# Optimization experiments

Hardware: AMD Instinct MI355X
Metric: run time of the kernel (lower is better)

Reference implementation:

```python
import jax, jax.numpy as jnp
import numpy as np

D_MODEL = 2048
N_HEADS = 8
HEAD_DIM = D_MODEL // N_HEADS
SCALING = HEAD_DIM ** -0.5


def setup_inputs() -> dict:
    key = jax.random.key(0)
    ks = jax.random.split(key, 9)
    B, S, D = 2, 2048, D_MODEL
    std = D ** -0.5
    inp = {"x": jax.random.normal(ks[0], (B, S, D), dtype=jnp.float32)}
    names = ["Wq", "Wk", "Wv", "Wo"]
    for i, n in enumerate(names):
        inp[n] = jax.random.normal(ks[1 + i], (D, D), dtype=jnp.float32) * std
        inp["b" + n[1]] = jax.random.normal(ks[5 + i], (D,), dtype=jnp.float32) * 0.01
    return inp


def reference(x, Wq, bq, Wk, bk, Wv, bv, Wo, bo):
    B, S, D = x.shape
    H, hd = N_HEADS, HEAD_DIM

    def proj(W, b):
        # nn.Linear: x @ W.T + b, then split heads -> [B, H, S, hd]
        y = jnp.einsum("bsd,ed->bse", x, W) + b
        return y.reshape(B, S, H, hd).transpose(0, 2, 1, 3)

    q = proj(Wq, bq)
    k = proj(Wk, bk)
    v = proj(Wv, bv)

    # scaled QK^T: [B, H, S, S]
    attn_weights = jnp.einsum("bhqd,bhkd->bhqk", q, k) * SCALING
    causal = jnp.tril(jnp.ones((S, S), dtype=bool))  # [S, S]
    attn_weights = jnp.where(causal[None, None], attn_weights, -jnp.inf)
    attn_probs = jax.nn.softmax(attn_weights, axis=-1)

    out = jnp.einsum("bhqk,bhkd->bhqd", attn_probs, v)  # [B, H, S, hd]
    out = out.transpose(0, 2, 1, 3).reshape(B, S, D)
    out = jnp.einsum("bsd,ed->bse", out, Wo) + bo
    return (out, attn_probs)
```

## Files before the change

kernel.cpp:

```cpp
#include <hip/hip_runtime.h>
#include <cstdint>
#include <cstddef>

typedef _Float16 f16;
typedef __attribute__((ext_vector_type(4))) _Float16 f16x4;
typedef __attribute__((ext_vector_type(8))) _Float16 f16x8;
typedef __attribute__((ext_vector_type(4))) float f32x4;

#define NB 2
#define SEQ 2048
#define DM 2048
#define NH 8
#define HD 256
#define MT (NB * SEQ)

#define QSCALE 0.09016844f
#define CEXP   23.08312065f

__device__ __forceinline__ void gload16(const f16* g, f16* l) {
    __builtin_amdgcn_global_load_lds(
        (const __attribute__((address_space(1))) uint32_t*)(const void*)g,
        (__attribute__((address_space(3))) uint32_t*)(void*)l,
        16, 0, 0);
}

__global__ __launch_bounds__(256) void k_cvt(const float* __restrict__ src,
                                             f16* __restrict__ dst, int n) {
    for (int i = (blockIdx.x * blockDim.x + threadIdx.x) * 4; i < n;
         i += gridDim.x * blockDim.x * 4) {
        f32x4 v = *(const f32x4*)(src + i);
        f16x4 h;
        h[0] = (f16)v[0]; h[1] = (f16)v[1]; h[2] = (f16)v[2]; h[3] = (f16)v[3];
        *(f16x4*)(dst + i) = h;
    }
}

__device__ __forceinline__ void stage6(const f16* __restrict__ A,
                                       const f16* __restrict__ B,
                                       int m0, int n0, int k0,
                                       f16* AL, f16* BL, int tid) {
#pragma unroll
    for (int j = 0; j < 4; ++j) {
        int flat = j * 4096 + tid * 8;
        int r = flat >> 6, c = flat & 63;
        int cs = c ^ ((r & 7) << 3);
        gload16(A + (size_t)(m0 + r) * DM + k0 + cs,
                AL + j * 4096 + (tid >> 6) * 512);
    }
#pragma unroll
    for (int j = 0; j < 2; ++j) {
        int flat = j * 4096 + tid * 8;
        int r = flat >> 6, c = flat & 63;
        int cs = c ^ ((r & 7) << 3);
        gload16(B + (size_t)(n0 + r) * DM + k0 + cs,
                BL + j * 4096 + (tid >> 6) * 512);
    }
}

__device__ __forceinline__ f16x8 rdfrag(const f16* buf, int rowbase, int lr,
                                        int lg, int kk) {
    int row = rowbase + lr;
    int c = (kk * 32 + lg * 8) ^ ((lr & 7) << 3);
    return *(const f16x8*)&buf[row * 64 + c];
}

__device__ __forceinline__ void gemm256x128_core(const f16* __restrict__ A,
                                                 const f16* __restrict__ B,
                                                 int m0, int n0,
                                                 f16* AL, f16* BL,
                                                 f32x4 acc[4][4]) {
    const int tid = threadIdx.x, wave = tid >> 6, lane = tid & 63;
    const int wm = wave >> 1, wn = wave & 1;
    const int lr = lane & 15, lg = lane >> 4;
    const int nt = DM / 64;

    stage6(A, B, m0, n0, 0, AL, BL, tid);
    stage6(A, B, m0, n0, 64, AL + 16384, BL + 8192, tid);

    for (int kt = 0; kt < nt; ++kt) {
        if (kt + 1 < nt) asm volatile("s_waitcnt vmcnt(6)" ::: "memory");
        else             asm volatile("s_waitcnt vmcnt(0)" ::: "memory");
        __builtin_amdgcn_s_barrier();
        __builtin_amdgcn_sched_barrier(0);

        const f16* Ab = AL + (kt % 3) * 16384;
        const f16* Bb = BL + (kt % 3) * 8192;
        const int arb = wm * 64, brb = wn * 64;

        f16x8 a0[2][2], b0[2][2];
#pragma unroll
        for (int mf = 0; mf < 2; ++mf)
#pragma unroll
            for (int kk = 0; kk < 2; ++kk)
                a0[mf][kk] = rdfrag(Ab, arb + mf * 16, lr, lg, kk);
#pragma unroll
        for (int nf = 0; nf < 2; ++nf)
#pragma unroll
            for (int kk = 0; kk < 2; ++kk)
                b0[nf][kk] = rdfrag(Bb, brb + nf * 16, lr, lg, kk);

        if (kt + 2 < nt)
            stage6(A, B, m0, n0, (kt + 2) * 64,
                   AL + ((kt + 2) % 3) * 16384, BL + ((kt + 2) % 3) * 8192, tid);

        __builtin_amdgcn_s_setprio(1);
#pragma unroll
        for (int mi = 0; mi < 2; ++mi)
#pragma unroll
            for (int nj = 0; nj < 2; ++nj)
#pragma unroll
                for (int kk = 0; kk < 2; ++kk)
                    acc[mi][nj] = __builtin_amdgcn_mfma_f32_16x16x32_f16(
                        a0[mi][kk], b0[nj][kk], acc[mi][nj], 0, 0, 0);
        __builtin_amdgcn_s_setprio(0);

        f16x8 b1[2][2];
#pragma unroll
        for (int nf = 0; nf < 2; ++nf)
#pragma unroll
            for (int kk = 0; kk < 2; ++kk)
                b1[nf][kk] = rdfrag(Bb, brb + 32 + nf * 16, lr, lg, kk);
        __builtin_amdgcn_s_setprio(1);
#pragma unroll
        for (int mi = 0; mi < 2; ++mi)
#pragma unroll
            for (int nj = 0; nj < 2; ++nj)
#pragma unroll
                for (int kk = 0; kk < 2; ++kk)
                    acc[mi][nj + 2] = __builtin_amdgcn_mfma_f32_16x16x32_f16(
                        a0[mi][kk], b1[nj][kk], acc[mi][nj + 2], 0, 0, 0);
        __builtin_amdgcn_s_setprio(0);

        f16x8 a1[2][2];
#pragma unroll
        for (int mf = 0; mf < 2; ++mf)
#pragma unroll
            for (int kk = 0; kk < 2; ++kk)
                a1[mf][kk] = rdfrag(Ab, arb + 32 + mf * 16, lr, lg, kk);
        __builtin_amdgcn_s_setprio(1);
#pragma unroll
        for (int mi = 0; mi < 2; ++mi)
#pragma unroll
            for (int nj = 0; nj < 2; ++nj)
#pragma unroll
                for (int kk = 0; kk < 2; ++kk)
                    acc[mi + 2][nj] = __builtin_amdgcn_mfma_f32_16x16x32_f16(
                        a1[mi][kk], b0[nj][kk], acc[mi + 2][nj], 0, 0, 0);
        __builtin_amdgcn_s_setprio(0);

        __builtin_amdgcn_s_setprio(1);
#pragma unroll
        for (int mi = 0; mi < 2; ++mi)
#pragma unroll
            for (int nj = 0; nj < 2; ++nj)
#pragma unroll
                for (int kk = 0; kk < 2; ++kk)
                    acc[mi + 2][nj + 2] = __builtin_amdgcn_mfma_f32_16x16x32_f16(
                        a1[mi][kk], b1[nj][kk], acc[mi + 2][nj + 2], 0, 0, 0);
        __builtin_amdgcn_s_setprio(0);
    }
}

__global__ __launch_bounds__(512, 1) void k_proj_qkv(
    const f16* __restrict__ xh, const f16* __restrict__ Wq,
    const f16* __restrict__ Wk, const f16* __restrict__ Wv,
    const float* __restrict__ bq, const float* __restrict__ bk,
    const float* __restrict__ bv,
    f16* __restrict__ Qh, f16* __restrict__ Kh, f16* __restrict__ Vth) {
    __shared__ __align__(16) f16 AL[3 * 16384];
    __shared__ __align__(16) f16 BL[3 * 8192];
    const int mode = blockIdx.z;
    const f16* W = (mode == 0) ? Wq : (mode == 1) ? Wk : Wv;
    const float* bias = (mode == 0) ? bq : (mode == 1) ? bk : bv;

    const int phys = blockIdx.x + 16 * blockIdx.y;
    const int xcdq = phys & 7, idx = phys >> 3;
    const int m0 = (xcdq * 2 + (idx >> 4)) * 256;
    const int n0 = (idx & 15) * 128;

    f32x4 acc[4][4];
#pragma unroll
    for (int mi = 0; mi < 4; ++mi)
#pragma unroll
        for (int nj = 0; nj < 4; ++nj) acc[mi][nj] = (f32x4){0.f, 0.f, 0.f, 0.f};

    gemm256x128_core(xh, W, m0, n0, AL, BL, acc);

    const int lane = threadIdx.x & 63, wave = threadIdx.x >> 6;
    const int wm = wave >> 1, wn = wave & 1;
    const int lr = lane & 15, lg = lane >> 4;
#pragma unroll
    for (int nj = 0; nj < 4; ++nj) {
        int n = n0 + wn * 64 + nj * 16 + lr;
        float bb = bias[n];
        int h = n >> 8, d = n & 255;
#pragma unroll
        for (int mi = 0; mi < 4; ++mi) {
#pragma unroll
            for (int i = 0; i < 4; ++i) {
                int m = m0 + wm * 64 + mi * 16 + lg * 4 + i;
                int b = m >> 11, s = m & 2047;
                float v = acc[mi][nj][i] + bb;
                size_t bh = (size_t)(b * NH + h);
                if (mode == 0)
                    Qh[((bh * SEQ + s) << 8) + d] = (f16)(v * QSCALE);
                else if (mode == 1)
                    Kh[((bh * SEQ + s) << 8) + d] = (f16)v;
                else
                    Vth[((bh * HD + d) << 11) + s] = (f16)v;
            }
        }
    }
}

__global__ __launch_bounds__(512, 1) void k_proj_o(
    const f16* __restrict__ Oh, const f16* __restrict__ Wo,
    const float* __restrict__ bo, float* __restrict__ out) {
    __shared__ __align__(16) f16 AL[3 * 16384];
    __shared__ __align__(16) f16 BL[3 * 8192];

    const int phys = blockIdx.x + 16 * blockIdx.y;
    const int xcdq = phys & 7, idx = phys >> 3;
    const int m0 = (xcdq * 2 + (idx >> 4)) * 256;
    const int n0 = (idx & 15) * 128;

    f32x4 acc[4][4];
#pragma unroll
    for (int mi = 0; mi < 4; ++mi)
#pragma unroll
        for (int nj = 0; nj < 4; ++nj) acc[mi][nj] = (f32x4){0.f, 0.f, 0.f, 0.f};

    gemm256x128_core(Oh, Wo, m0, n0, AL, BL, acc);

    const int lane = threadIdx.x & 63, wave = threadIdx.x >> 6;
    const int wm = wave >> 1, wn = wave & 1;
    const int lr = lane & 15, lg = lane >> 4;
#pragma unroll
    for (int nj = 0; nj < 4; ++nj) {
        int n = n0 + wn * 64 + nj * 16 + lr;
        float bb = bo[n];
#pragma unroll
        for (int mi = 0; mi < 4; ++mi) {
#pragma unroll
            for (int i = 0; i < 4; ++i) {
                int m = m0 + wm * 64 + mi * 16 + lg * 4 + i;
                out[(size_t)m * DM + n] = acc[mi][nj][i] + bb;
            }
        }
    }
}

__device__ __forceinline__ void stageK(const f16* __restrict__ Kb, int kt,
                                       f16* buf, int wave, int lane) {
#pragma unroll
    for (int j = 0; j < 8; ++j) {
        int base = (j * 4 + wave) << 9;
        int flat = base + (lane << 3);
        int r = flat >> 8;
        int c = (flat & 255) ^ ((r & 7) << 3);
        gload16(Kb + (size_t)(kt * 64 + r) * HD + c, buf + base);
    }
}
__device__ __forceinline__ void stageV(const f16* __restrict__ Vb, int kt,
                                       f16* buf, int wave, int lane) {
#pragma unroll
    for (int j = 0; j < 8; ++j) {
        int base = (j * 4 + wave) << 9;
        int flat = base + (lane << 3);
        int rv = flat >> 6;
        int cv = (flat & 63) ^ ((rv & 3) << 3);
        gload16(Vb + ((size_t)rv << 11) + kt * 64 + cv, buf + base);
    }
}

__global__ __launch_bounds__(256, 2) void k_attn(
    const f16* __restrict__ Qh, const f16* __restrict__ Kh,
    const f16* __restrict__ Vth, float* __restrict__ P,
    f16* __restrict__ Oh) {
    __shared__ __align__(16) f16 B0[64 * 256];
    __shared__ __align__(16) f16 B1[64 * 256];
    __shared__ __align__(16) f16 Ps[4][16][72];

    const int bid = blockIdx.x;
    const int xcd = bid & 7;
    const int slot = bid >> 3;
    const int psel = slot >> 5;
    const int s5 = slot & 31;
    const int qb = psel ? s5 : (31 - s5);
    const int bhid = xcd * 2 + psel;
    const int b = bhid >> 3, h = bhid & 7;

    const int q0 = qb * 64;
    const int tid = threadIdx.x, wave = tid >> 6, lane = tid & 63;
    const int lr = lane & 15, lg = lane >> 4;
    const size_t bh = (size_t)bhid;
    const f16* Qb = Qh + (bh << 19);
    const f16* Kb = Kh + (bh << 19);
    const f16* Vb = Vth + (bh << 19);
    float* Pb = P + (bh << 22);

    const int kswz = (lr & 7) << 3;
    const int vswz = (lr & 3) << 3;

    f16x8 aq[8];
    {
        const f16* qrow = Qb + (size_t)(q0 + wave * 16 + lr) * HD + lg * 8;
#pragma unroll
        for (int kk = 0; kk < 8; ++kk) aq[kk] = *(const f16x8*)(qrow + kk * 32);
    }

    const int rowb = q0 + wave * 16 + lg * 4;
    const int nt = qb + 1;

    float psum[4] = {0.f, 0.f, 0.f, 0.f};

    stageK(Kb, 0, B0, wave, lane);
    for (int kt = 0; kt < nt; ++kt) {
        f16* cur = (kt & 1) ? B1 : B0;
        f16* nxt = (kt & 1) ? B0 : B1;
        if (kt + 1 < nt) {
            stageK(Kb, kt + 1, nxt, wave, lane);
            asm volatile("s_waitcnt vmcnt(8)" ::: "memory");
        } else {
            asm volatile("s_waitcnt vmcnt(0)" ::: "memory");
        }
        __builtin_amdgcn_s_barrier();
        __builtin_amdgcn_sched_barrier(0);

        f32x4 s[4];
#pragma unroll
        for (int nj = 0; nj < 4; ++nj) s[nj] = (f32x4){0.f, 0.f, 0.f, 0.f};
        __builtin_amdgcn_s_setprio(1);
#pragma unroll
        for (int kk = 0; kk < 8; ++kk) {
#pragma unroll
            for (int nj = 0; nj < 4; ++nj) {
                f16x8 bk = *(const f16x8*)&cur[(nj * 16 + lr) * 256 +
                                               ((kk * 32 + lg * 8) ^ kswz)];
                s[nj] = __builtin_amdgcn_mfma_f32_16x16x32_f16(aq[kk], bk, s[nj], 0, 0, 0);
            }
        }
        __builtin_amdgcn_s_setprio(0);
        const int colb = kt * 64 + lr;
#pragma unroll
        for (int i = 0; i < 4; ++i) {
            int row = rowb + i;
#pragma unroll
            for (int nj = 0; nj < 4; ++nj)
                psum[i] += (colb + nj * 16 <= row) ? exp2f(s[nj][i] - CEXP) : 0.f;
        }
        asm volatile("" ::: "memory");
        __builtin_amdgcn_s_barrier();
        __builtin_amdgcn_sched_barrier(0);
    }

    float inv[4];
#pragma unroll
    for (int i = 0; i < 4; ++i) {
        float l = psum[i];
        l += __shfl_xor(l, 1);
        l += __shfl_xor(l, 2);
        l += __shfl_xor(l, 4);
        l += __shfl_xor(l, 8);
        inv[i] = 1.f / l;
    }

    f32x4 o[16];
#pragma unroll
    for (int n = 0; n < 16; ++n) o[n] = (f32x4){0.f, 0.f, 0.f, 0.f};

    stageK(Kb, 0, B0, wave, lane);
    for (int kt = 0; kt < nt; ++kt) {
        stageV(Vb, kt, B1, wave, lane);
        asm volatile("s_waitcnt vmcnt(8)" ::: "memory");
        __builtin_amdgcn_s_barrier();
        __builtin_amdgcn_sched_barrier(0);

        f32x4 s[4];
#pragma unroll
        for (int nj = 0; nj < 4; ++nj) s[nj] = (f32x4){0.f, 0.f, 0.f, 0.f};
        __builtin_amdgcn_s_setprio(1);
#pragma unroll
        for (int kk = 0; kk < 8; ++kk) {
#pragma unroll
            for (int nj = 0; nj < 4; ++nj) {
                f16x8 bk = *(const f16x8*)&B0[(nj * 16 + lr) * 256 +
                                              ((kk * 32 + lg * 8) ^ kswz)];
                s[nj] = __builtin_amdgcn_mfma_f32_16x16x32_f16(aq[kk], bk, s[nj], 0, 0, 0);
            }
        }
        __builtin_amdgcn_s_setprio(0);
#pragma unroll
        for (int i = 0; i < 4; ++i) {
            int row = rowb + i;
#pragma unroll
            for (int nj = 0; nj < 4; ++nj) {
                int col = kt * 64 + nj * 16 + lr;
                float pv = (col <= row) ? exp2f(s[nj][i] - CEXP) * inv[i] : 0.f;
                Ps[wave][lg * 4 + i][nj * 16 + lr] = (f16)pv;
            }
        }
        asm volatile("s_waitcnt vmcnt(0)" ::: "memory");
        __builtin_amdgcn_s_barrier();
        __builtin_amdgcn_sched_barrier(0);

        if (kt + 1 < nt) stageK(Kb, kt + 1, B0, wave, lane);

#pragma unroll
        for (int h2 = 0; h2 < 2; ++h2) {
            int rr = h2 * 8 + (lane >> 3);
            int cc = (lane & 7) * 8;
            f16x8 ph = *(const f16x8*)&Ps[wave][rr][cc];
            int row = q0 + wave * 16 + rr;
            float* dst = Pb + (size_t)row * SEQ + kt * 64 + cc;
            f32x4 lo = {(float)ph[0], (float)ph[1], (float)ph[2], (float)ph[3]};
            f32x4 hi = {(float)ph[4], (float)ph[5], (float)ph[6], (float)ph[7]};
            *(f32x4*)dst = lo;
            *(f32x4*)(dst + 4) = hi;
        }

        __builtin_amdgcn_s_setprio(1);
#pragma unroll
        for (int kk2 = 0; kk2 < 2; ++kk2) {
            f16x8 pa = *(const f16x8*)&Ps[wave][lr][kk2 * 32 + lg * 8];
#pragma unroll
            for (int n = 0; n < 16; ++n) {
                f16x8 bv = *(const f16x8*)&B1[(n * 16 + lr) * 64 +
                                              ((kk2 * 32 + lg * 8) ^ vswz)];
                o[n] = __builtin_amdgcn_mfma_f32_16x16x32_f16(pa, bv, o[n], 0, 0, 0);
            }
        }
        __builtin_amdgcn_s_setprio(0);
        asm volatile("" ::: "memory");
        __builtin_amdgcn_s_barrier();
        __builtin_amdgcn_sched_barrier(0);
    }

    int kstart = (qb + 1) * 64;
    if (kstart < SEQ) {
        f32x4 z = (f32x4){0.f, 0.f, 0.f, 0.f};
        for (int r = 0; r < 64; ++r) {
            float* rp = Pb + (size_t)(q0 + r) * SEQ;
            for (int c = kstart + tid * 4; c < SEQ; c += 1024)
                *(f32x4*)(rp + c) = z;
        }
    }

#pragma unroll
    for (int n = 0; n < 16; ++n) {
#pragma unroll
        for (int i = 0; i < 4; ++i) {
            int row = rowb + i;
            int d = n * 16 + lr;
            Oh[((size_t)b * SEQ + row) * DM + h * HD + d] = (f16)o[n][i];
        }
    }
}

extern "C" void kernel_launch(void* const* d_in, const int* in_sizes, int n_in,
                              void* d_out, int out_size, void* d_ws, size_t ws_size,
                              hipStream_t stream) {
    const float* x  = (const float*)d_in[0];
    const float* Wq = (const float*)d_in[1];
    const float* bq = (const float*)d_in[2];
    const float* Wk = (const float*)d_in[3];
    const float* bk = (const float*)d_in[4];
    const float* Wv = (const float*)d_in[5];
    const float* bv = (const float*)d_in[6];
    const float* Wo = (const float*)d_in[7];
    const float* bo = (const float*)d_in[8];

    float* out  = (float*)d_out;
    float* Pout = out + (size_t)MT * DM;

    f16* xh  = (f16*)Pout;
    f16* Wqh = xh + (size_t)MT * DM;
    f16* Wkh = Wqh + (size_t)DM * DM;
    f16* Wvh = Wkh + (size_t)DM * DM;

    f16* ws16 = (f16*)d_ws;
    f16* Woh = ws16;
    f16* Qh  = Woh + (size_t)DM * DM;
    f16* Kh  = Qh + (size_t)8388608;
    f16* Vth = Kh + (size_t)8388608;
    f16* Oh  = Vth + (size_t)8388608;
    if (ws_size < (size_t)(4194304 + 4 * 8388608) * sizeof(f16)) return;

    k_cvt<<<2048, 256, 0, stream>>>(x, xh, MT * DM);
    k_cvt<<<1024, 256, 0, stream>>>(Wq, Wqh, DM * DM);
    k_cvt<<<1024, 256, 0, stream>>>(Wk, Wkh, DM * DM);
    k_cvt<<<1024, 256, 0, stream>>>(Wv, Wvh, DM * DM);
    k_cvt<<<1024, 256, 0, stream>>>(Wo, Woh, DM * DM);

    dim3 g1(DM / 128, MT / 256, 3);
    k_proj_qkv<<<g1, 512, 0, stream>>>(xh, Wqh, Wkh, Wvh, bq, bk, bv, Qh, Kh, Vth);

    k_attn<<<dim3(512), 256, 0, stream>>>(Qh, Kh, Vth, Pout, Oh);

    dim3 g3(DM / 128, MT / 256, 1);
    k_proj_o<<<g3, 512, 0, stream>>>(Oh, Woh, bo, out);
}
```

Before: 371.9 us.

## Restructure GEMM main loop into two k-phases and reorder PV before P store

The projection GEMM inner loop now runs as two k-half phases. Each phase loads 4x4 fragments, issues half of the next tile's global-to-LDS loads, then runs 16 MFMAs between extra barriers, in a ping-pong style schedule. In the attention kernel the PV MFMA block moves ahead of the probability global stores, and the vmcnt wait is loosened so that stores can stay in flight. This aims to overlap memory traffic with MFMA work, at the cost of extra barriers per iteration.

After: 359.2 us. 3.4% less time.

```diff
diff --git a/kernel.cpp b/kernel.cpp
--- a/kernel.cpp
+++ b/kernel.cpp
@@ -35,20 +35,21 @@
     }
 }
 
-__device__ __forceinline__ void stage6(const f16* __restrict__ A,
+__device__ __forceinline__ void stage3(const f16* __restrict__ A,
                                        const f16* __restrict__ B,
                                        int m0, int n0, int k0,
-                                       f16* AL, f16* BL, int tid) {
-#pragma unroll
-    for (int j = 0; j < 4; ++j) {
+                                       f16* AL, f16* BL, int tid, int half) {
+#pragma unroll
+    for (int jj = 0; jj < 2; ++jj) {
+        int j = half * 2 + jj;
         int flat = j * 4096 + tid * 8;
         int r = flat >> 6, c = flat & 63;
         int cs = c ^ ((r & 7) << 3);
         gload16(A + (size_t)(m0 + r) * DM + k0 + cs,
                 AL + j * 4096 + (tid >> 6) * 512);
     }
-#pragma unroll
-    for (int j = 0; j < 2; ++j) {
+    {
+        int j = half;
         int flat = j * 4096 + tid * 8;
         int r = flat >> 6, c = flat & 63;
         int cs = c ^ ((r & 7) << 3);
@@ -74,8 +75,10 @@
     const int lr = lane & 15, lg = lane >> 4;
     const int nt = DM / 64;
 
-    stage6(A, B, m0, n0, 0, AL, BL, tid);
-    stage6(A, B, m0, n0, 64, AL + 16384, BL + 8192, tid);
+    stage3(A, B, m0, n0, 0, AL, BL, tid, 0);
+    stage3(A, B, m0, n0, 0, AL, BL, tid, 1);
+    stage3(A, B, m0, n0, 64, AL + 16384, BL + 8192, tid, 0);
+    stage3(A, B, m0, n0, 64, AL + 16384, BL + 8192, tid, 1);
 
     for (int kt = 0; kt < nt; ++kt) {
         if (kt + 1 < nt) asm volatile("s_waitcnt vmcnt(6)" ::: "memory");
@@ -87,77 +90,36 @@
         const f16* Bb = BL + (kt % 3) * 8192;
         const int arb = wm * 64, brb = wn * 64;
 
-        f16x8 a0[2][2], b0[2][2];
-#pragma unroll
-        for (int mf = 0; mf < 2; ++mf)
-#pragma unroll
-            for (int kk = 0; kk < 2; ++kk)
-                a0[mf][kk] = rdfrag(Ab, arb + mf * 16, lr, lg, kk);
-#pragma unroll
-        for (int nf = 0; nf < 2; ++nf)
-#pragma unroll
-            for (int kk = 0; kk < 2; ++kk)
-                b0[nf][kk] = rdfrag(Bb, brb + nf * 16, lr, lg, kk);
-
-        if (kt + 2 < nt)
-            stage6(A, B, m0, n0, (kt + 2) * 64,
-                   AL + ((kt + 2) % 3) * 16384, BL + ((kt + 2) % 3) * 8192, tid);
-
-        __builtin_amdgcn_s_setprio(1);
-#pragma unroll
-        for (int mi = 0; mi < 2; ++mi)
-#pragma unroll
-            for (int nj = 0; nj < 2; ++nj)
-#pragma unroll
-                for (int kk = 0; kk < 2; ++kk)
+#pragma unroll
+        for (int ph = 0; ph < 2; ++ph) {
+            f16x8 af[4], bf[4];
+#pragma unroll
+            for (int mf = 0; mf < 4; ++mf)
+                af[mf] = rdfrag(Ab, arb + mf * 16, lr, lg, ph);
+#pragma unroll
+            for (int nf = 0; nf < 4; ++nf)
+                bf[nf] = rdfrag(Bb, brb + nf * 16, lr, lg, ph);
+
+            if (kt + 2 < nt)
+                stage3(A, B, m0, n0, (kt + 2) * 64,
+                       AL + ((kt + 2) % 3) * 16384,
+                       BL + ((kt + 2) % 3) * 8192, tid, ph);
+
+            __builtin_amdgcn_sched_barrier(0);
+            __builtin_amdgcn_s_barrier();
+            asm volatile("s_waitcnt lgkmcnt(0)" ::: "memory");
+            __builtin_amdgcn_sched_barrier(0);
+
+            __builtin_amdgcn_s_setprio(1);
+#pragma unroll
+            for (int mi = 0; mi < 4; ++mi)
+#pragma unroll
+                for (int nj = 0; nj < 4; ++nj)
                     acc[mi][nj] = __builtin_amdgcn_mfma_f32_16x16x32_f16(
-                        a0[mi][kk], b0[nj][kk], acc[mi][nj], 0, 0, 0);
-        __builtin_amdgcn_s_setprio(0);
-
-        f16x8 b1[2][2];
-#pragma unroll
-        for (int nf = 0; nf < 2; ++nf)
-#pragma unroll
-            for (int kk = 0; kk < 2; ++kk)
-                b1[nf][kk] = rdfrag(Bb, brb + 32 + nf * 16, lr, lg, kk);
-        __builtin_amdgcn_s_setprio(1);
-#pragma unroll
-        for (int mi = 0; mi < 2; ++mi)
-#pragma unroll
-            for (int nj = 0; nj < 2; ++nj)
-#pragma unroll
-                for (int kk = 0; kk < 2; ++kk)
-                    acc[mi][nj + 2] = __builtin_amdgcn_mfma_f32_16x16x32_f16(
-                        a0[mi][kk], b1[nj][kk], acc[mi][nj + 2], 0, 0, 0);
-        __builtin_amdgcn_s_setprio(0);
-
-        f16x8 a1[2][2];
-#pragma unroll
-        for (int mf = 0; mf < 2; ++mf)
-#pragma unroll
-            for (int kk = 0; kk < 2; ++kk)
-                a1[mf][kk] = rdfrag(Ab, arb + 32 + mf * 16, lr, lg, kk);
-        __builtin_amdgcn_s_setprio(1);
-#pragma unroll
-        for (int mi = 0; mi < 2; ++mi)
-#pragma unroll
-            for (int nj = 0; nj < 2; ++nj)
-#pragma unroll
-                for (int kk = 0; kk < 2; ++kk)
-                    acc[mi + 2][nj] = __builtin_amdgcn_mfma_f32_16x16x32_f16(
-                        a1[mi][kk], b0[nj][kk], acc[mi + 2][nj], 0, 0, 0);
-        __builtin_amdgcn_s_setprio(0);
-
-        __builtin_amdgcn_s_setprio(1);
-#pragma unroll
-        for (int mi = 0; mi < 2; ++mi)
-#pragma unroll
-            for (int nj = 0; nj < 2; ++nj)
-#pragma unroll
-                for (int kk = 0; kk < 2; ++kk)
-                    acc[mi + 2][nj + 2] = __builtin_amdgcn_mfma_f32_16x16x32_f16(
-                        a1[mi][kk], b1[nj][kk], acc[mi + 2][nj + 2], 0, 0, 0);
-        __builtin_amdgcn_s_setprio(0);
+                        af[mi], bf[nj], acc[mi][nj], 0, 0, 0);
+            __builtin_amdgcn_s_setprio(0);
+            __builtin_amdgcn_s_barrier();
+        }
     }
 }
 
@@ -372,7 +334,8 @@
     stageK(Kb, 0, B0, wave, lane);
     for (int kt = 0; kt < nt; ++kt) {
         stageV(Vb, kt, B1, wave, lane);
-        asm volatile("s_waitcnt vmcnt(8)" ::: "memory");
+        if (kt == 0) asm volatile("s_waitcnt vmcnt(8)" ::: "memory");
+        else         asm volatile("s_waitcnt vmcnt(10)" ::: "memory");
         __builtin_amdgcn_s_barrier();
         __builtin_amdgcn_sched_barrier(0);
 
@@ -405,6 +368,19 @@
         __builtin_amdgcn_sched_barrier(0);
 
         if (kt + 1 < nt) stageK(Kb, kt + 1, B0, wave, lane);
+
+        __builtin_amdgcn_s_setprio(1);
+#pragma unroll
+        for (int kk2 = 0; kk2 < 2; ++kk2) {
+            f16x8 pa = *(const f16x8*)&Ps[wave][lr][kk2 * 32 + lg * 8];
+#pragma unroll
+            for (int n = 0; n < 16; ++n) {
+                f16x8 bv = *(const f16x8*)&B1[(n * 16 + lr) * 64 +
+                                              ((kk2 * 32 + lg * 8) ^ vswz)];
+                o[n] = __builtin_amdgcn_mfma_f32_16x16x32_f16(pa, bv, o[n], 0, 0, 0);
+            }
+        }
+        __builtin_amdgcn_s_setprio(0);
 
 #pragma unroll
         for (int h2 = 0; h2 < 2; ++h2) {
@@ -419,18 +395,6 @@
             *(f32x4*)(dst + 4) = hi;
         }
 
-        __builtin_amdgcn_s_setprio(1);
-#pragma unroll
-        for (int kk2 = 0; kk2 < 2; ++kk2) {
-            f16x8 pa = *(const f16x8*)&Ps[wave][lr][kk2 * 32 + lg * 8];
-#pragma unroll
-            for (int n = 0; n < 16; ++n) {
-                f16x8 bv = *(const f16x8*)&B1[(n * 16 + lr) * 64 +
-                                              ((kk2 * 32 + lg * 8) ^ vswz)];
-                o[n] = __builtin_amdgcn_mfma_f32_16x16x32_f16(pa, bv, o[n], 0, 0, 0);
-            }
-        }
-        __builtin_amdgcn_s_setprio(0);
         asm volatile("" ::: "memory");
         __builtin_amdgcn_s_barrier();
         __builtin_amdgcn_sched_barrier(0);
```
